# Optimization experiments

Hardware: AMD Instinct MI355X
Metric: run time of the kernel (lower is better)

The kernel has to match this reference:

```python
import jax, jax.numpy as jnp
import numpy as np

KLD_SCALE = 10.0
COMMIT_COST = 0.25


def setup_inputs() -> dict:
    key = jax.random.key(0)
    k1, k2, k3, k4 = jax.random.split(key, 4)
    B, C, T = 32, 512, 4096
    D, K = 128, 1024
    z = jax.random.normal(k1, (B, C, T), dtype=jnp.float32)
    proj_w = jax.random.normal(k2, (D, C), dtype=jnp.float32) * (1.0 / np.sqrt(C))
    proj_b = jax.random.normal(k3, (D,), dtype=jnp.float32) * 0.01
    embed_w = jax.random.normal(k4, (K, D), dtype=jnp.float32)
    return {"z": z, "proj_w": proj_w, "proj_b": proj_b, "embed_w": embed_w}


def reference(z, proj_w, proj_b, embed_w):
    B, C, T = z.shape
    D = proj_w.shape[0]
    # 1x1 Conv1d == per-timestep linear: [B,C,T] x [D,C] -> [B,T,D]
    z_e = jnp.einsum('bct,dc->btd', z, proj_w) + proj_b
    flat = z_e.reshape(-1, D)  # [B*T, D]
    # squared euclidean distances to codebook: [B*T, K]
    dist = (jnp.sum(flat * flat, axis=1, keepdims=True)
            - 2.0 * (flat @ embed_w.T)
            + jnp.sum(embed_w * embed_w, axis=1)[None, :])
    ind = jnp.argmin(dist, axis=1).reshape(B, T)  # == argmax(-dist)
    z_q = embed_w[ind]  # [B,T,D] codebook gather
    sg = jax.lax.stop_gradient
    diff = KLD_SCALE * (COMMIT_COST * jnp.mean((sg(z_q) - z_e) ** 2)
                        + jnp.mean((z_q - sg(z_e)) ** 2))
    z_q_ste = z_e + sg(z_q - z_e)  # straight-through estimator
    z_q_out = jnp.transpose(z_q_ste, (0, 2, 1))  # [B,D,T]
    return z_q_out, diff, ind
```

## Files before the change

kernel.cpp:

```cpp
#include <hip/hip_runtime.h>

#define B_N 32
#define C_N 512
#define T_N 4096
#define D_N 128
#define K_N 1024
#define N_N (B_N * T_N)

typedef _Float16 f16x8 __attribute__((ext_vector_type(8)));
typedef float    f32x4 __attribute__((ext_vector_type(4)));

#define ZSWZ_OFF 0
#define ESWZ_OFF 67108864
#define ENS_OFF  67895296
#define WSWZ_OFF 68431872
#define PART_OFF 68694016

#define GLL(g, s) __builtin_amdgcn_global_load_lds( \
    (const __attribute__((address_space(1))) unsigned int*)(g), \
    (__attribute__((address_space(3))) unsigned int*)(s), 16, 0, 0)

__global__ __launch_bounds__(128) void k_eprep(const float* __restrict__ E,
                                               _Float16* __restrict__ eswz,
                                               float* __restrict__ ens) {
  __shared__ float s2[2];
  const int code = blockIdx.x, d = threadIdx.x;
  const float e  = E[(size_t)code * D_N + d];
  const float es = e * 64.f;
  const _Float16 eh = (_Float16)es;
  const _Float16 el = (_Float16)(es - (float)eh);

  float sq = es * es;
  #pragma unroll
  for (int off = 32; off > 0; off >>= 1) sq += __shfl_down(sq, off);
  if ((d & 63) == 0) s2[d >> 6] = sq;
  __syncthreads();
  if (d == 0) ens[code] = s2[0] + s2[1];

  const int kt = code >> 7, mi = (code >> 4) & 7, lrow = code & 15;
  const int lk = (d >> 3) & 3, i = d & 7, cb = d >> 5;
  const size_t tile = (size_t)kt * 12;
  #define PUT(c, v) eswz[(((tile + (c)) * 512 + mi * 64 + lk * 16 + lrow) << 3) + i] = (v)
  PUT(cb, eh);
  PUT(4 + cb, el);
  PUT(8 + cb, eh);
  #undef PUT
}

__global__ __launch_bounds__(256) void k_wprep(const float* __restrict__ W,
                                               _Float16* __restrict__ wswz) {
  const int e = blockIdx.x * 256 + threadIdx.x;
  const int d = e >> 9, c = e & 511;
  const float x = W[d * C_N + c] * 8.f;
  const _Float16 h  = (_Float16)x;
  const _Float16 lo = (_Float16)(x - (float)h);
  const int kc = c >> 5, gg = (c >> 3) & 3, j = c & 7;
  const int nf = d >> 4, ll = gg * 16 + (d & 15);
  const size_t base = (size_t)kc * 8192 + ((size_t)nf * 64 + ll) * 8 + j;
  wswz[base]        = h;
  wswz[base + 4096] = lo;
}

__global__ __launch_bounds__(256, 2) void k_projm(const float* __restrict__ z,
                                                  const _Float16* __restrict__ wswz,
                                                  const float* __restrict__ bias,
                                                  f16x8* __restrict__ zswz) {
  __shared__ __align__(16) char lds[65536];

  const int tid = threadIdx.x;
  const int l   = tid & 63, w = tid >> 6;
  const int g   = l >> 4, li = l & 15;
  const int b   = blockIdx.y, t0 = blockIdx.x * 128;
  const float* zb = z + (size_t)b * C_N * T_N + t0;

  float bs[8];
  #pragma unroll
  for (int nf = 0; nf < 8; ++nf) bs[nf] = bias[nf * 16 + li] * 64.f;

  f32x4 acc[2][8];
  #pragma unroll
  for (int mi = 0; mi < 2; ++mi)
    #pragma unroll
    for (int nf = 0; nf < 8; ++nf) acc[mi][nf] = (f32x4)0.f;

  auto stage = [&](int kc, int buf) {
    char* zdst = lds + buf * 16384;
    char* wdst = lds + 32768 + buf * 16384;
    #pragma unroll
    for (int s = 0; s < 4; ++s) {
      const int q = w * 4 + s;
      const unsigned v = q * 64 + l;
      const unsigned u = v ^ (((v >> 8) & 1) << 2);
      GLL((const char*)zb +
              ((size_t)(kc * 32 + (u >> 5)) * T_N + (size_t)(u & 31) * 4) * 4,
          zdst + q * 1024);
      GLL((const char*)wswz + (size_t)kc * 16384 + q * 1024 + l * 16,
          wdst + q * 1024);
    }
  };

  stage(0, 0);
  __syncthreads();

  int buf = 0;
  for (int kc = 0; kc < 16; ++kc) {
    if (kc + 1 < 16) stage(kc + 1, buf ^ 1);

    const float* zl = (const float*)(lds + buf * 16384);
    const f16x8* wb = (const f16x8*)(lds + 32768 + buf * 16384);

    f16x8 ah[2], al[2];
    #pragma unroll
    for (int mi = 0; mi < 2; ++mi) {
      const int mt = w * 2 + mi;
      const int a0 = (g * 1024 + mt * 16 + li) ^ ((g & 1) << 4);
      #pragma unroll
      for (int j = 0; j < 8; ++j) {
        const float x = zl[a0 + j * 128] * 8.f;
        const _Float16 h = (_Float16)x;
        ah[mi][j] = h;
        al[mi][j] = (_Float16)(x - (float)h);
      }
    }
    f16x8 bh[8], bl[8];
    #pragma unroll
    for (int nf = 0; nf < 8; ++nf) {
      bh[nf] = wb[nf * 64 + l];
      bl[nf] = wb[512 + nf * 64 + l];
    }
    #pragma unroll
    for (int mi = 0; mi < 2; ++mi)
      #pragma unroll
      for (int nf = 0; nf < 8; ++nf) {
        acc[mi][nf] = __builtin_amdgcn_mfma_f32_16x16x32_f16(ah[mi], bh[nf], acc[mi][nf], 0, 0, 0);
        acc[mi][nf] = __builtin_amdgcn_mfma_f32_16x16x32_f16(al[mi], bh[nf], acc[mi][nf], 0, 0, 0);
        acc[mi][nf] = __builtin_amdgcn_mfma_f32_16x16x32_f16(ah[mi], bl[nf], acc[mi][nf], 0, 0, 0);
      }
    __syncthreads();
    buf ^= 1;
  }

  unsigned* cs = (unsigned*)lds;
  const int n0 = b * T_N + t0;
  for (int p = 0; p < 2; ++p) {
    #pragma unroll
    for (int mi = 0; mi < 2; ++mi) {
      const int trow = (w * 2 + mi) * 16 + g * 4;
      #pragma unroll
      for (int nfl = 0; nfl < 4; ++nfl) {
        const int nf = p * 4 + nfl;
        #pragma unroll
        for (int r = 0; r < 4; ++r) {
          const float x = acc[mi][nf][r] + bs[nf];
          const _Float16 h  = (_Float16)x;
          const _Float16 lo = (_Float16)(x - (float)h);
          cs[(trow + r) * 68 + nfl * 16 + li] =
              (unsigned)__builtin_bit_cast(unsigned short, h) |
              ((unsigned)__builtin_bit_cast(unsigned short, lo) << 16);
        }
      }
    }
    __syncthreads();
    #pragma unroll
    for (int i = 0; i < 4; ++i) {
      const int u = i * 256 + tid;
      const int t = u & 127, dc = u >> 7;
      f16x8 vh, vl;
      #pragma unroll
      for (int e = 0; e < 8; ++e) {
        const unsigned vv = cs[t * 68 + dc * 8 + e];
        vh[e] = __builtin_bit_cast(_Float16, (unsigned short)(vv & 0xffff));
        vl[e] = __builtin_bit_cast(_Float16, (unsigned short)(vv >> 16));
      }
      const int n = n0 + t;
      const int cu = p * 2 + (dc >> 2), lk = dc & 3;
      const size_t idx = ((size_t)(n >> 4) * 8 + cu) * 64 + lk * 16 + (n & 15);
      zswz[idx]       = vh;
      zswz[idx + 256] = vl;
    }
    __syncthreads();
  }
}

template<int NF0>
__device__ __forceinline__ float gather_reg(int wc, int l, const int* skf,
                                            const float* E, float* ob,
                                            const f16x8 (&bfr)[8][4]) {
  float psum = 0.f;
  #pragma unroll
  for (int nl = 0; nl < 2; ++nl) {
    constexpr int NFA[2] = {NF0, NF0 + 1};
    const int nf = NFA[nl];
    const int r = wc * 64 + nf * 16 + (l & 15);
    const int k = skf[r];
    const float* Er = E + (size_t)k * D_N;
    #pragma unroll
    for (int cu = 0; cu < 4; ++cu) {
      const int d0 = cu * 32 + (l >> 4) * 8;
      const float4 e0 = *(const float4*)(Er + d0);
      const float4 e1 = *(const float4*)(Er + d0 + 4);
      const float ev[8] = {e0.x, e0.y, e0.z, e0.w, e1.x, e1.y, e1.z, e1.w};
      const f16x8 hi = bfr[cu][nf];
      const f16x8 lo = bfr[cu + 4][nf];
      #pragma unroll
      for (int j = 0; j < 8; ++j) {
        const float ze = ((float)hi[j] + (float)lo[j]) * 0.015625f;
        const float df = ev[j] - ze;
        psum += df * df;
        ob[(size_t)(d0 + j) * T_N + r] = ev[j];
      }
    }
  }
  return psum;
}

__global__ __launch_bounds__(256, 2) void k_argmin4(const f16x8* __restrict__ zswz,
                                                    const f16x8* __restrict__ eswz,
                                                    const float* __restrict__ ens,
                                                    const float* __restrict__ E,
                                                    float* __restrict__ out,
                                                    float* __restrict__ indf,
                                                    float* __restrict__ part) {
  __shared__ __align__(16) char sbuf[65536];
  __shared__ float sdl[256];
  __shared__ int   skl[256];
  __shared__ int   skf[128];

  const int tid = threadIdx.x, l = tid & 63, w = tid >> 6;
  const int wr = w >> 1, wc = w & 1;
  const int blk = blockIdx.x;

  const char* zsrc = (const char*)zswz + (size_t)blk * 65536;
  #pragma unroll
  for (int s = 0; s < 16; ++s)
    GLL(zsrc + s * 4096 + tid * 16, sbuf + s * 4096 + w * 1024);
  asm volatile("s_waitcnt vmcnt(0)" ::: "memory");
  __syncthreads();

  f16x8 bfr[8][4];
  #pragma unroll
  for (int cu = 0; cu < 8; ++cu)
    #pragma unroll
    for (int nf = 0; nf < 4; ++nf)
      bfr[cu][nf] =
          *(const f16x8*)(sbuf + (((((wc * 4 + nf) * 8 + cu) * 64) + l) << 4));
  __syncthreads();

  const char* easrc = (const char*)eswz;
  #pragma unroll
  for (int s = 0; s < 4; ++s) {
    GLL(easrc + s * 8192 + tid * 16,        sbuf + s * 8192 + w * 1024);
    GLL(easrc + s * 8192 + 4096 + tid * 16, sbuf + s * 8192 + 4096 + w * 1024);
  }

  float bestd[4];
  int   bestk[4];
  #pragma unroll
  for (int nf = 0; nf < 4; ++nf) { bestd[nf] = 3.4e38f; bestk[nf] = 0; }

  for (int kt = 0; kt < 8; ++kt) {
    f32x4 acc[4][4];
    #pragma unroll
    for (int mi = 0; mi < 4; ++mi)
      #pragma unroll
      for (int nf = 0; nf < 4; ++nf) acc[mi][nf] = (f32x4)0.f;

    #pragma unroll
    for (int pp = 0; pp < 3; ++pp) {
      const int p = kt * 3 + pp;
      char* rbuf = sbuf + (size_t)(p & 1) * 32768;
      char* wbufp = sbuf + (size_t)((p + 1) & 1) * 32768;

      __syncthreads();

      if (p + 1 < 24) {
        const size_t nb = (size_t)(p + 1) * 32768;
        #pragma unroll
        for (int s = 0; s < 4; ++s) {
          GLL(easrc + nb + s * 8192 + tid * 16,
              wbufp + s * 8192 + w * 1024);
          GLL(easrc + nb + s * 8192 + 4096 + tid * 16,
              wbufp + s * 8192 + 4096 + w * 1024);
        }
      }

      #pragma unroll
      for (int j = 0; j < 4; ++j) {
        constexpr int CUMAP[12] = {0, 1, 2, 3, 0, 1, 2, 3, 4, 5, 6, 7};
        const int c  = pp * 4 + j;
        const int cu = CUMAP[c];
        f16x8 afr[4];
        #pragma unroll
        for (int mi = 0; mi < 4; ++mi)
          afr[mi] = *(const f16x8*)(rbuf + (size_t)j * 8192 +
                                    (((wr * 4 + mi) * 64 + l) << 4));
        #pragma unroll
        for (int mi = 0; mi < 4; ++mi)
          #pragma unroll
          for (int nf = 0; nf < 4; ++nf)
            acc[mi][nf] = __builtin_amdgcn_mfma_f32_16x16x32_f16(
                afr[mi], bfr[cu][nf], acc[mi][nf], 0, 0, 0);
      }
    }

    #pragma unroll
    for (int mi = 0; mi < 4; ++mi) {
      const int cbase = kt * 128 + wr * 64 + mi * 16 + ((l >> 4) << 2);
      const float4 e4 = *(const float4*)&ens[cbase];
      const float ev[4] = {e4.x, e4.y, e4.z, e4.w};
      #pragma unroll
      for (int r = 0; r < 4; ++r) {
        const int k = cbase + r;
        #pragma unroll
        for (int nf = 0; nf < 4; ++nf) {
          const float dv = ev[r] - 2.0f * acc[mi][nf][r];
          if (dv < bestd[nf]) { bestd[nf] = dv; bestk[nf] = k; }
        }
      }
    }
  }

  #pragma unroll
  for (int nf = 0; nf < 4; ++nf) {
    float d = bestd[nf]; int k = bestk[nf];
    #pragma unroll
    for (int off = 16; off < 64; off <<= 1) {
      const float od = __shfl_xor(d, off);
      const int   ok = __shfl_xor(k, off);
      if (od < d || (od == d && ok < k)) { d = od; k = ok; }
    }
    if (l < 16) {
      sdl[wr * 128 + wc * 64 + nf * 16 + l] = d;
      skl[wr * 128 + wc * 64 + nf * 16 + l] = k;
    }
  }
  __syncthreads();
  if (tid < 128) {
    float d0 = sdl[tid], d1 = sdl[128 + tid];
    int   k0 = skl[tid], k1 = skl[128 + tid];
    if (d1 < d0 || (d1 == d0 && k1 < k0)) { d0 = d1; k0 = k1; }
    skf[tid] = k0;
    indf[blk * 128 + tid] = (float)k0;
  }
  __syncthreads();

  const int b  = blk >> 5;
  const int t0 = (blk & 31) << 7;
  float* ob = out + (size_t)b * (D_N * T_N) + t0;
  float psum = (wr == 0) ? gather_reg<0>(wc, l, skf, E, ob, bfr)
                         : gather_reg<2>(wc, l, skf, E, ob, bfr);
  #pragma unroll
  for (int off = 32; off > 0; off >>= 1) psum += __shfl_xor(psum, off);
  if (l == 0) part[blk * 4 + w] = psum;
}

__global__ __launch_bounds__(256) void k_diff(const float* __restrict__ part,
                                              float* __restrict__ diff_out) {
  __shared__ double wsd[4];
  const int tid = threadIdx.x;
  double s = 0.0;
  for (int i = tid; i < 4096; i += 256) s += (double)part[i];
  #pragma unroll
  for (int off = 32; off > 0; off >>= 1) s += __shfl_down(s, off);
  if ((tid & 63) == 0) wsd[tid >> 6] = s;
  __syncthreads();
  if (tid == 0) {
    const double tot = wsd[0] + wsd[1] + wsd[2] + wsd[3];
    diff_out[0] = (float)(12.5 * tot / (double)((size_t)N_N * D_N));
  }
}

extern "C" void kernel_launch(void* const* d_in, const int* in_sizes, int n_in,
                              void* d_out, int out_size, void* d_ws, size_t ws_size,
                              hipStream_t stream) {
  const float* z    = (const float*)d_in[0];
  const float* W    = (const float*)d_in[1];
  const float* bias = (const float*)d_in[2];
  const float* E    = (const float*)d_in[3];

  float* out = (float*)d_out;
  float* out_q    = out;
  float* out_diff = out + 16777216;
  float* out_ind  = out + 16777217;

  char* ws = (char*)d_ws;
  f16x8*    zswz = (f16x8*)(ws + ZSWZ_OFF);
  _Float16* eswz = (_Float16*)(ws + ESWZ_OFF);
  float*    ens  = (float*)(ws + ENS_OFF);
  _Float16* wswz = (_Float16*)(ws + WSWZ_OFF);
  float*    part = (float*)(ws + PART_OFF);

  k_eprep<<<K_N, 128, 0, stream>>>(E, eswz, ens);
  k_wprep<<<256, 256, 0, stream>>>(W, wswz);
  k_projm<<<dim3(T_N / 128, B_N), 256, 0, stream>>>(z, wswz, bias, zswz);
  k_argmin4<<<N_N / 128, 256, 0, stream>>>(zswz, (const f16x8*)eswz, ens, E,
                                           out_q, out_ind, part);
  k_diff<<<1, 256, 0, stream>>>(part, out_diff);
}
```

Before: 214.8 us.

## Read codebook fragments directly from global memory instead of LDS double buffering

```diff
diff --git a/kernel.cpp b/kernel.cpp
--- a/kernel.cpp
+++ b/kernel.cpp
@@ -214,7 +214,7 @@
   return psum;
 }
 
-__global__ __launch_bounds__(256, 2) void k_argmin4(const f16x8* __restrict__ zswz,
+__global__ __launch_bounds__(256, 2) void k_argmin5(const f16x8* __restrict__ zswz,
                                                     const f16x8* __restrict__ eswz,
                                                     const float* __restrict__ ens,
                                                     const float* __restrict__ E,
@@ -246,12 +246,7 @@
           *(const f16x8*)(sbuf + (((((wc * 4 + nf) * 8 + cu) * 64) + l) << 4));
   __syncthreads();
 
-  const char* easrc = (const char*)eswz;
-  #pragma unroll
-  for (int s = 0; s < 4; ++s) {
-    GLL(easrc + s * 8192 + tid * 16,        sbuf + s * 8192 + w * 1024);
-    GLL(easrc + s * 8192 + 4096 + tid * 16, sbuf + s * 8192 + 4096 + w * 1024);
-  }
+  const char* easrc = (const char*)eswz + (size_t)wr * 4096;
 
   float bestd[4];
   int   bestk[4];
@@ -266,41 +261,20 @@
       for (int nf = 0; nf < 4; ++nf) acc[mi][nf] = (f32x4)0.f;
 
     #pragma unroll
-    for (int pp = 0; pp < 3; ++pp) {
-      const int p = kt * 3 + pp;
-      char* rbuf = sbuf + (size_t)(p & 1) * 32768;
-      char* wbufp = sbuf + (size_t)((p + 1) & 1) * 32768;
-
-      __syncthreads();
-
-      if (p + 1 < 24) {
-        const size_t nb = (size_t)(p + 1) * 32768;
+    for (int c = 0; c < 12; ++c) {
+      constexpr int CUMAP[12] = {0, 1, 2, 3, 0, 1, 2, 3, 4, 5, 6, 7};
+      const int cu = CUMAP[c];
+      f16x8 afr[4];
+      #pragma unroll
+      for (int mi = 0; mi < 4; ++mi)
+        afr[mi] = *(const f16x8*)(easrc + (size_t)(kt * 12 + c) * 8192 +
+                                  ((mi * 64 + l) << 4));
+      #pragma unroll
+      for (int mi = 0; mi < 4; ++mi)
         #pragma unroll
-        for (int s = 0; s < 4; ++s) {
-          GLL(easrc + nb + s * 8192 + tid * 16,
-              wbufp + s * 8192 + w * 1024);
-          GLL(easrc + nb + s * 8192 + 4096 + tid * 16,
-              wbufp + s * 8192 + 4096 + w * 1024);
-        }
-      }
-
-      #pragma unroll
-      for (int j = 0; j < 4; ++j) {
-        constexpr int CUMAP[12] = {0, 1, 2, 3, 0, 1, 2, 3, 4, 5, 6, 7};
-        const int c  = pp * 4 + j;
-        const int cu = CUMAP[c];
-        f16x8 afr[4];
-        #pragma unroll
-        for (int mi = 0; mi < 4; ++mi)
-          afr[mi] = *(const f16x8*)(rbuf + (size_t)j * 8192 +
-                                    (((wr * 4 + mi) * 64 + l) << 4));
-        #pragma unroll
-        for (int mi = 0; mi < 4; ++mi)
-          #pragma unroll
-          for (int nf = 0; nf < 4; ++nf)
-            acc[mi][nf] = __builtin_amdgcn_mfma_f32_16x16x32_f16(
-                afr[mi], bfr[cu][nf], acc[mi][nf], 0, 0, 0);
-      }
+        for (int nf = 0; nf < 4; ++nf)
+          acc[mi][nf] = __builtin_amdgcn_mfma_f32_16x16x32_f16(
+              afr[mi], bfr[cu][nf], acc[mi][nf], 0, 0, 0);
     }
 
     #pragma unroll
@@ -393,7 +367,7 @@
   k_eprep<<<K_N, 128, 0, stream>>>(E, eswz, ens);
   k_wprep<<<256, 256, 0, stream>>>(W, wswz);
   k_projm<<<dim3(T_N / 128, B_N), 256, 0, stream>>>(z, wswz, bias, zswz);
-  k_argmin4<<<N_N / 128, 256, 0, stream>>>(zswz, (const f16x8*)eswz, ens, E,
+  k_argmin5<<<N_N / 128, 256, 0, stream>>>(zswz, (const f16x8*)eswz, ens, E,
                                            out_q, out_ind, part);
   k_diff<<<1, 256, 0, stream>>>(part, out_diff);
 }
```

New measurement: 251.8 us. +17.2%, slower.
